# Optimization experiments

Hardware: AMD Instinct MI355X
Metric: run time of the kernel (lower is better)

The kernel has to match this reference:

```python
import jax, jax.numpy as jnp
from jax import lax
import numpy as np

T, B, D, H = 1024, 512, 128, 128  # time steps, batch, input dim, hidden size


def setup_inputs() -> dict:
    key = jax.random.key(0)
    ks = jax.random.split(key, 8)
    s_fc = 1.0 / np.sqrt(D)
    s_gru = 1.0 / np.sqrt(H)
    return {
        "x": jax.random.normal(ks[0], (T, B, D), dtype=jnp.float32),
        "W1": jax.random.uniform(ks[1], (128, D), jnp.float32, -s_fc, s_fc),
        "b1": jax.random.uniform(ks[2], (128,), jnp.float32, -s_fc, s_fc),
        "W_ih": jax.random.uniform(ks[3], (3 * H, 128), jnp.float32, -s_gru, s_gru),
        "W_hh": jax.random.uniform(ks[4], (3 * H, H), jnp.float32, -s_gru, s_gru),
        "b_ih": jax.random.uniform(ks[5], (3 * H,), jnp.float32, -s_gru, s_gru),
        "b_hh": jax.random.uniform(ks[6], (3 * H,), jnp.float32, -s_gru, s_gru),
    }


def reference(x, W1, b1, W_ih, W_hh, b_ih, b_hh):
    # fc1 applied to every step (batched once over T*B for efficiency)
    feats = jnp.einsum('tbd,hd->tbh', x, W1) + b1  # [T, B, 128]

    hidden = W_hh.shape[1]

    def step(h, f):
        # PyTorch GRUCell gate math
        gi = f @ W_ih.T + b_ih          # [B, 3H]
        gh = h @ W_hh.T + b_hh          # [B, 3H]
        i_r, i_z, i_n = jnp.split(gi, 3, axis=-1)
        h_r, h_z, h_n = jnp.split(gh, 3, axis=-1)
        r = jax.nn.sigmoid(i_r + h_r)
        z = jax.nn.sigmoid(i_z + h_z)
        n = jnp.tanh(i_n + r * h_n)
        h_new = (1.0 - z) * n + z * h
        return h_new, None

    # first call gru(feats) passes no hidden -> zeros initial state
    h0 = jnp.zeros((x.shape[1], hidden), dtype=x.dtype)
    h_final, _ = lax.scan(step, h0, feats)
    return h_final  # [B, H]
```

## Files before the change

### kernel.cpp

```cpp
#include <hip/hip_runtime.h>
#include <hip/hip_bf16.h>

#define T_STEPS 1024
#define BATCH   512
#define DIM     128
#define G3      384
#define NCHUNK  (T_STEPS/8)

typedef __attribute__((ext_vector_type(8))) short bf16x8;
typedef __attribute__((ext_vector_type(4))) float f32x4;

__device__ __forceinline__ short f2bf(float f) {
  unsigned u = __builtin_bit_cast(unsigned, f);
  u += 0x7FFFu + ((u >> 16) & 1u);
  return (short)(u >> 16);
}

__device__ __forceinline__ void block_sync_lds() {
  asm volatile("s_waitcnt lgkmcnt(0)\n\ts_barrier" ::: "memory");
}

__global__ void prep_kernel(const float* __restrict__ W1, const float* __restrict__ b1,
                            const float* __restrict__ W_ih, const float* __restrict__ W_hh,
                            const float* __restrict__ b_ih,
                            short* __restrict__ wc_bf, short* __restrict__ whh_bf,
                            float* __restrict__ bc) {
  const int g = blockIdx.x;
  const int d = threadIdx.x;
  float acc = 0.f;
  #pragma unroll 4
  for (int k = 0; k < 128; ++k)
    acc = fmaf(W_ih[g * 128 + k], W1[k * 128 + d], acc);
  wc_bf[g * 128 + d]  = f2bf(acc);
  whh_bf[g * 128 + d] = f2bf(W_hh[g * 128 + d]);

  __shared__ float red[128];
  red[d] = W_ih[g * 128 + d] * b1[d];
  __syncthreads();
  #pragma unroll
  for (int s = 64; s > 0; s >>= 1) {
    if (d < s) red[d] += red[d + s];
    __syncthreads();
  }
  if (d == 0) bc[g] = red[0] + b_ih[g];
}

__device__ __forceinline__ float gate_h(float gir, float giz, float gin,
                                        float ghr, float ghz, float ghn,
                                        float bhn, float hp) {
  const float r = __builtin_amdgcn_rcpf(1.f + __expf(-(gir + ghr)));
  const float z = __builtin_amdgcn_rcpf(1.f + __expf(-(giz + ghz)));
  float nv = gin + r * (ghn + bhn);
  nv = fminf(fmaxf(nv, -15.f), 15.f);
  const float e = __expf(2.f * nv);
  const float n = 1.f - 2.f * __builtin_amdgcn_rcpf(e + 1.f);
  return z * (hp - n) + n;
}

__global__ __launch_bounds__(512, 2) void gru_kernel(
    const float* __restrict__ x,
    const float* __restrict__ b_hh,
    const short* __restrict__ wc_bf,
    const short* __restrict__ whh_bf,
    const float* __restrict__ bc,
    float* __restrict__ out)
{
  const int tid = threadIdx.x;
  const int w   = tid >> 6;
  const int l   = tid & 63;
  const int q   = l >> 4;
  const int c   = l & 15;
  const int b0  = blockIdx.x * 2;

  __shared__ f32x4 gi4[2][16][128];
  __shared__ short hbuf[2][2][128];

  const f32x4 zero4 = {0.f, 0.f, 0.f, 0.f};

  if (w < 4) {
    const int half = q & 1;
    const int ch   = q >> 1;
    const int colX = w * 32 + (half << 4) + c;

    bf16x8 Bh[3][2][4];
    #pragma unroll
    for (int g = 0; g < 3; ++g)
      #pragma unroll
      for (int Tt = 0; Tt < 2; ++Tt)
        #pragma unroll
        for (int kt = 0; kt < 4; ++kt)
          Bh[g][Tt][kt] = *(const bf16x8*)(whh_bf +
              (g * 128 + w * 32 + Tt * 16 + c) * 128 + kt * 32 + q * 8);
    const float bhn = b_hh[256 + colX];

    ((short*)hbuf)[tid] = 0;
    float hp = 0.f;
    __syncthreads();

    const short* hb0 = &hbuf[0][c >> 3][q * 8];
    const short* hb1 = &hbuf[1][c >> 3][q * 8];

    for (int cc = 0; cc < NCHUNK; ++cc) {
      f32x4 gi[8];
      {
        const f32x4* gp = &gi4[cc & 1][ch][colX];
        #pragma unroll
        for (int s = 0; s < 8; ++s) gi[s] = gp[2 * s * 128];
      }
      #pragma unroll
      for (int s = 0; s < 8; ++s) {
        const short* hb = (s & 1) ? hb1 : hb0;
        bf16x8 Ah[4];
        #pragma unroll
        for (int kt = 0; kt < 4; ++kt)
          Ah[kt] = *(const bf16x8*)(hb + kt * 32);

        f32x4 a0[3] = {zero4, zero4, zero4};
        f32x4 a1[3] = {zero4, zero4, zero4};
        #pragma unroll
        for (int kt = 0; kt < 4; ++kt)
          #pragma unroll
          for (int g = 0; g < 3; ++g) {
            a0[g] = __builtin_amdgcn_mfma_f32_16x16x32_bf16(Ah[kt], Bh[g][0][kt], a0[g], 0, 0, 0);
            a1[g] = __builtin_amdgcn_mfma_f32_16x16x32_bf16(Ah[kt], Bh[g][1][kt], a1[g], 0, 0, 0);
          }
        const float ghr = half ? a1[0][0] : a0[0][0];
        const float ghz = half ? a1[1][0] : a0[1][0];
        const float ghn = half ? a1[2][0] : a0[2][0];
        const float h = gate_h(gi[s][0], gi[s][1], gi[s][2], ghr, ghz, ghn, bhn, hp);
        hp = h;
        hbuf[(s & 1) ^ 1][ch][colX] = f2bf(h);
        block_sync_lds();
      }
    }
    out[(size_t)(b0 + ch) * DIM + colX] = hp;
  } else {
    const int w4 = w - 4;
    const int jg0 = w4 * 32 + c, jg1 = jg0 + 16;
    bf16x8 Bc[3][2][4];
    #pragma unroll
    for (int g = 0; g < 3; ++g)
      #pragma unroll
      for (int Tt = 0; Tt < 2; ++Tt)
        #pragma unroll
        for (int kt = 0; kt < 4; ++kt)
          Bc[g][Tt][kt] = *(const bf16x8*)(wc_bf +
              (g * 128 + w4 * 32 + Tt * 16 + c) * 128 + kt * 32 + q * 8);
    const float fr0 = bc[jg0]       + b_hh[jg0];
    const float fz0 = bc[128 + jg0] + b_hh[128 + jg0];
    const float fn0 = bc[256 + jg0];
    const float fr1 = bc[jg1]       + b_hh[jg1];
    const float fz1 = bc[128 + jg1] + b_hh[128 + jg1];
    const float fn1 = bc[256 + jg1];

    const int trel = c >> 1, chn = c & 1;
    f32x4 xv[8];

    {
      const float* xb = x + ((size_t)trel * BATCH + (b0 + chn)) * DIM + q * 8;
      f32x4 xt[8];
      #pragma unroll
      for (int kt = 0; kt < 4; ++kt) {
        xt[2 * kt]     = *(const f32x4*)(xb + kt * 32);
        xt[2 * kt + 1] = *(const f32x4*)(xb + kt * 32 + 4);
      }
      bf16x8 Ax[4];
      #pragma unroll
      for (int kt = 0; kt < 4; ++kt) {
        const f32x4 v0 = xt[2 * kt], v1 = xt[2 * kt + 1];
        bf16x8 a;
        a[0] = f2bf(v0[0]); a[1] = f2bf(v0[1]); a[2] = f2bf(v0[2]); a[3] = f2bf(v0[3]);
        a[4] = f2bf(v1[0]); a[5] = f2bf(v1[1]); a[6] = f2bf(v1[2]); a[7] = f2bf(v1[3]);
        Ax[kt] = a;
      }
      f32x4 ga[2][3] = {{zero4, zero4, zero4}, {zero4, zero4, zero4}};
      #pragma unroll
      for (int kt = 0; kt < 4; ++kt)
        #pragma unroll
        for (int g = 0; g < 3; ++g) {
          ga[0][g] = __builtin_amdgcn_mfma_f32_16x16x32_bf16(Ax[kt], Bc[g][0][kt], ga[0][g], 0, 0, 0);
          ga[1][g] = __builtin_amdgcn_mfma_f32_16x16x32_bf16(Ax[kt], Bc[g][1][kt], ga[1][g], 0, 0, 0);
        }
      #pragma unroll
      for (int r = 0; r < 4; ++r) {
        f32x4 vA = {ga[0][0][r] + fr0, ga[0][1][r] + fz0, ga[0][2][r] + fn0, 0.f};
        f32x4 vB = {ga[1][0][r] + fr1, ga[1][1][r] + fz1, ga[1][2][r] + fn1, 0.f};
        gi4[0][4 * q + r][jg0] = vA;
        gi4[0][4 * q + r][jg1] = vB;
      }
      const float* xb1 = x + ((size_t)(8 + trel) * BATCH + (b0 + chn)) * DIM + q * 8;
      #pragma unroll
      for (int kt = 0; kt < 4; ++kt) {
        xv[2 * kt]     = *(const f32x4*)(xb1 + kt * 32);
        xv[2 * kt + 1] = *(const f32x4*)(xb1 + kt * 32 + 4);
      }
    }
    __syncthreads();

    for (int cc = 0; cc < NCHUNK; ++cc) {
      const int tc = cc + 1;
      bf16x8 Ax[4];
      f32x4 ga[2][3];
      #pragma unroll
      for (int s = 0; s < 8; ++s) {
        if (tc < NCHUNK) {
          if (s == 0) {
            #pragma unroll
            for (int kt = 0; kt < 4; ++kt) {
              const f32x4 v0 = xv[2 * kt], v1 = xv[2 * kt + 1];
              bf16x8 a;
              a[0] = f2bf(v0[0]); a[1] = f2bf(v0[1]); a[2] = f2bf(v0[2]); a[3] = f2bf(v0[3]);
              a[4] = f2bf(v1[0]); a[5] = f2bf(v1[1]); a[6] = f2bf(v1[2]); a[7] = f2bf(v1[3]);
              Ax[kt] = a;
            }
            #pragma unroll
            for (int Tt = 0; Tt < 2; ++Tt)
              #pragma unroll
              for (int g = 0; g < 3; ++g) ga[Tt][g] = zero4;
          } else if (s <= 4) {
            const int kt = s - 1;
            #pragma unroll
            for (int g = 0; g < 3; ++g) {
              ga[0][g] = __builtin_amdgcn_mfma_f32_16x16x32_bf16(Ax[kt], Bc[g][0][kt], ga[0][g], 0, 0, 0);
              ga[1][g] = __builtin_amdgcn_mfma_f32_16x16x32_bf16(Ax[kt], Bc[g][1][kt], ga[1][g], 0, 0, 0);
            }
          } else if (s == 5) {
            if (tc + 1 < NCHUNK) {
              const float* xb = x + ((size_t)((tc + 1) * 8 + trel) * BATCH + (b0 + chn)) * DIM + q * 8;
              #pragma unroll
              for (int kt = 0; kt < 4; ++kt) {
                xv[2 * kt]     = *(const f32x4*)(xb + kt * 32);
                xv[2 * kt + 1] = *(const f32x4*)(xb + kt * 32 + 4);
              }
            }
          } else if (s == 6) {
            #pragma unroll
            for (int r = 0; r < 4; ++r) {
              ga[0][0][r] += fr0; ga[0][1][r] += fz0; ga[0][2][r] += fn0;
              ga[1][0][r] += fr1; ga[1][1][r] += fz1; ga[1][2][r] += fn1;
            }
          } else {
            const int nbuf = tc & 1;
            #pragma unroll
            for (int r = 0; r < 4; ++r) {
              f32x4 vA = {ga[0][0][r], ga[0][1][r], ga[0][2][r], 0.f};
              f32x4 vB = {ga[1][0][r], ga[1][1][r], ga[1][2][r], 0.f};
              gi4[nbuf][4 * q + r][jg0] = vA;
              gi4[nbuf][4 * q + r][jg1] = vB;
            }
          }
        }
        block_sync_lds();
      }
    }
  }
}

extern "C" void kernel_launch(void* const* d_in, const int* in_sizes, int n_in,
                              void* d_out, int out_size, void* d_ws, size_t ws_size,
                              hipStream_t stream) {
  const float* x    = (const float*)d_in[0];
  const float* W1   = (const float*)d_in[1];
  const float* b1   = (const float*)d_in[2];
  const float* W_ih = (const float*)d_in[3];
  const float* W_hh = (const float*)d_in[4];
  const float* b_ih = (const float*)d_in[5];
  const float* b_hh = (const float*)d_in[6];
  float* out = (float*)d_out;

  char* ws = (char*)d_ws;
  short* wc_bf  = (short*)(ws);
  short* whh_bf = (short*)(ws + 98304);
  float* bc     = (float*)(ws + 196608);

  prep_kernel<<<dim3(G3), dim3(128), 0, stream>>>(W1, b1, W_ih, W_hh, b_ih, wc_bf, whh_bf, bc);
  gru_kernel<<<dim3(BATCH / 2), dim3(512), 0, stream>>>(x, b_hh, wc_bf, whh_bf, bc, out);
}
```

Measured before the change: 687.5 us.

## Fold log2e scaling into weights, split MFMA chains, pad LDS, raise recurrent priority

```diff
diff --git a/kernel.cpp b/kernel.cpp
--- a/kernel.cpp
+++ b/kernel.cpp
@@ -6,9 +6,14 @@
 #define DIM     128
 #define G3      384
 #define NCHUNK  (T_STEPS/8)
+#define GI_STRIDE 129
 
 typedef __attribute__((ext_vector_type(8))) short bf16x8;
 typedef __attribute__((ext_vector_type(4))) float f32x4;
+
+#define LOG2E  1.44269504f
+#define LOG2E2 2.88539008f
+#define NV_CLAMP 43.28f
 
 __device__ __forceinline__ short f2bf(float f) {
   unsigned u = __builtin_bit_cast(unsigned, f);
@@ -22,17 +27,18 @@
 
 __global__ void prep_kernel(const float* __restrict__ W1, const float* __restrict__ b1,
                             const float* __restrict__ W_ih, const float* __restrict__ W_hh,
-                            const float* __restrict__ b_ih,
+                            const float* __restrict__ b_ih, const float* __restrict__ b_hh,
                             short* __restrict__ wc_bf, short* __restrict__ whh_bf,
-                            float* __restrict__ bc) {
+                            float* __restrict__ bc, float* __restrict__ bhh_s) {
   const int g = blockIdx.x;
   const int d = threadIdx.x;
+  const float sg = (g < 256) ? LOG2E : LOG2E2;
   float acc = 0.f;
   #pragma unroll 4
   for (int k = 0; k < 128; ++k)
     acc = fmaf(W_ih[g * 128 + k], W1[k * 128 + d], acc);
-  wc_bf[g * 128 + d]  = f2bf(acc);
-  whh_bf[g * 128 + d] = f2bf(W_hh[g * 128 + d]);
+  wc_bf[g * 128 + d]  = f2bf(acc * sg);
+  whh_bf[g * 128 + d] = f2bf(W_hh[g * 128 + d] * sg);
 
   __shared__ float red[128];
   red[d] = W_ih[g * 128 + d] * b1[d];
@@ -42,24 +48,15 @@
     if (d < s) red[d] += red[d + s];
     __syncthreads();
   }
-  if (d == 0) bc[g] = red[0] + b_ih[g];
-}
-
-__device__ __forceinline__ float gate_h(float gir, float giz, float gin,
-                                        float ghr, float ghz, float ghn,
-                                        float bhn, float hp) {
-  const float r = __builtin_amdgcn_rcpf(1.f + __expf(-(gir + ghr)));
-  const float z = __builtin_amdgcn_rcpf(1.f + __expf(-(giz + ghz)));
-  float nv = gin + r * (ghn + bhn);
-  nv = fminf(fmaxf(nv, -15.f), 15.f);
-  const float e = __expf(2.f * nv);
-  const float n = 1.f - 2.f * __builtin_amdgcn_rcpf(e + 1.f);
-  return z * (hp - n) + n;
+  if (d == 0) {
+    bc[g]    = (red[0] + b_ih[g]) * sg;
+    bhh_s[g] = b_hh[g] * sg;
+  }
 }
 
 __global__ __launch_bounds__(512, 2) void gru_kernel(
     const float* __restrict__ x,
-    const float* __restrict__ b_hh,
+    const float* __restrict__ bhh_s,
     const short* __restrict__ wc_bf,
     const short* __restrict__ whh_bf,
     const float* __restrict__ bc,
@@ -72,7 +69,7 @@
   const int c   = l & 15;
   const int b0  = blockIdx.x * 2;
 
-  __shared__ f32x4 gi4[2][16][128];
+  __shared__ f32x4 gi4[2 * 16 * GI_STRIDE];
   __shared__ short hbuf[2][2][128];
 
   const f32x4 zero4 = {0.f, 0.f, 0.f, 0.f};
@@ -91,7 +88,7 @@
         for (int kt = 0; kt < 4; ++kt)
           Bh[g][Tt][kt] = *(const bf16x8*)(whh_bf +
               (g * 128 + w * 32 + Tt * 16 + c) * 128 + kt * 32 + q * 8);
-    const float bhn = b_hh[256 + colX];
+    const float bhn = bhh_s[256 + colX];
 
     ((short*)hbuf)[tid] = 0;
     float hp = 0.f;
@@ -100,12 +97,13 @@
     const short* hb0 = &hbuf[0][c >> 3][q * 8];
     const short* hb1 = &hbuf[1][c >> 3][q * 8];
 
+    __builtin_amdgcn_s_setprio(1);
     for (int cc = 0; cc < NCHUNK; ++cc) {
       f32x4 gi[8];
       {
-        const f32x4* gp = &gi4[cc & 1][ch][colX];
-        #pragma unroll
-        for (int s = 0; s < 8; ++s) gi[s] = gp[2 * s * 128];
+        const f32x4* gp = gi4 + (cc & 1) * (16 * GI_STRIDE) + ch * GI_STRIDE + colX;
+        #pragma unroll
+        for (int s = 0; s < 8; ++s) gi[s] = gp[2 * s * GI_STRIDE];
       }
       #pragma unroll
       for (int s = 0; s < 8; ++s) {
@@ -115,24 +113,49 @@
         for (int kt = 0; kt < 4; ++kt)
           Ah[kt] = *(const bf16x8*)(hb + kt * 32);
 
-        f32x4 a0[3] = {zero4, zero4, zero4};
-        f32x4 a1[3] = {zero4, zero4, zero4};
-        #pragma unroll
-        for (int kt = 0; kt < 4; ++kt)
-          #pragma unroll
-          for (int g = 0; g < 3; ++g) {
-            a0[g] = __builtin_amdgcn_mfma_f32_16x16x32_bf16(Ah[kt], Bh[g][0][kt], a0[g], 0, 0, 0);
-            a1[g] = __builtin_amdgcn_mfma_f32_16x16x32_bf16(Ah[kt], Bh[g][1][kt], a1[g], 0, 0, 0);
-          }
-        const float ghr = half ? a1[0][0] : a0[0][0];
-        const float ghz = half ? a1[1][0] : a0[1][0];
-        const float ghn = half ? a1[2][0] : a0[2][0];
-        const float h = gate_h(gi[s][0], gi[s][1], gi[s][2], ghr, ghz, ghn, bhn, hp);
+        f32x4 r0A = __builtin_amdgcn_mfma_f32_16x16x32_bf16(Ah[0], Bh[0][0][0], zero4, 0, 0, 0);
+        f32x4 r1A = __builtin_amdgcn_mfma_f32_16x16x32_bf16(Ah[0], Bh[0][1][0], zero4, 0, 0, 0);
+        f32x4 r0B = __builtin_amdgcn_mfma_f32_16x16x32_bf16(Ah[2], Bh[0][0][2], zero4, 0, 0, 0);
+        f32x4 r1B = __builtin_amdgcn_mfma_f32_16x16x32_bf16(Ah[2], Bh[0][1][2], zero4, 0, 0, 0);
+        r0A = __builtin_amdgcn_mfma_f32_16x16x32_bf16(Ah[1], Bh[0][0][1], r0A, 0, 0, 0);
+        r1A = __builtin_amdgcn_mfma_f32_16x16x32_bf16(Ah[1], Bh[0][1][1], r1A, 0, 0, 0);
+        r0B = __builtin_amdgcn_mfma_f32_16x16x32_bf16(Ah[3], Bh[0][0][3], r0B, 0, 0, 0);
+        r1B = __builtin_amdgcn_mfma_f32_16x16x32_bf16(Ah[3], Bh[0][1][3], r1B, 0, 0, 0);
+        f32x4 z0A = __builtin_amdgcn_mfma_f32_16x16x32_bf16(Ah[0], Bh[1][0][0], zero4, 0, 0, 0);
+        f32x4 z1A = __builtin_amdgcn_mfma_f32_16x16x32_bf16(Ah[0], Bh[1][1][0], zero4, 0, 0, 0);
+        f32x4 z0B = __builtin_amdgcn_mfma_f32_16x16x32_bf16(Ah[2], Bh[1][0][2], zero4, 0, 0, 0);
+        f32x4 z1B = __builtin_amdgcn_mfma_f32_16x16x32_bf16(Ah[2], Bh[1][1][2], zero4, 0, 0, 0);
+        z0A = __builtin_amdgcn_mfma_f32_16x16x32_bf16(Ah[1], Bh[1][0][1], z0A, 0, 0, 0);
+        z1A = __builtin_amdgcn_mfma_f32_16x16x32_bf16(Ah[1], Bh[1][1][1], z1A, 0, 0, 0);
+        z0B = __builtin_amdgcn_mfma_f32_16x16x32_bf16(Ah[3], Bh[1][0][3], z0B, 0, 0, 0);
+        z1B = __builtin_amdgcn_mfma_f32_16x16x32_bf16(Ah[3], Bh[1][1][3], z1B, 0, 0, 0);
+
+        const float ghr = half ? (r1A[0] + r1B[0]) : (r0A[0] + r0B[0]);
+        const float ghz = half ? (z1A[0] + z1B[0]) : (z0A[0] + z0B[0]);
+        const float rg = __builtin_amdgcn_rcpf(1.f + __builtin_amdgcn_exp2f(-(gi[s][0] + ghr)));
+        const float zg = __builtin_amdgcn_rcpf(1.f + __builtin_amdgcn_exp2f(-(gi[s][1] + ghz)));
+
+        f32x4 n0A = __builtin_amdgcn_mfma_f32_16x16x32_bf16(Ah[0], Bh[2][0][0], zero4, 0, 0, 0);
+        f32x4 n1A = __builtin_amdgcn_mfma_f32_16x16x32_bf16(Ah[0], Bh[2][1][0], zero4, 0, 0, 0);
+        f32x4 n0B = __builtin_amdgcn_mfma_f32_16x16x32_bf16(Ah[2], Bh[2][0][2], zero4, 0, 0, 0);
+        f32x4 n1B = __builtin_amdgcn_mfma_f32_16x16x32_bf16(Ah[2], Bh[2][1][2], zero4, 0, 0, 0);
+        n0A = __builtin_amdgcn_mfma_f32_16x16x32_bf16(Ah[1], Bh[2][0][1], n0A, 0, 0, 0);
+        n1A = __builtin_amdgcn_mfma_f32_16x16x32_bf16(Ah[1], Bh[2][1][1], n1A, 0, 0, 0);
+        n0B = __builtin_amdgcn_mfma_f32_16x16x32_bf16(Ah[3], Bh[2][0][3], n0B, 0, 0, 0);
+        n1B = __builtin_amdgcn_mfma_f32_16x16x32_bf16(Ah[3], Bh[2][1][3], n1B, 0, 0, 0);
+        const float ghn = half ? (n1A[0] + n1B[0]) : (n0A[0] + n0B[0]);
+
+        float nv = gi[s][2] + rg * (ghn + bhn);
+        nv = fminf(fmaxf(nv, -NV_CLAMP), NV_CLAMP);
+        const float e  = __builtin_amdgcn_exp2f(nv);
+        const float nn = 1.f - 2.f * __builtin_amdgcn_rcpf(e + 1.f);
+        const float h  = zg * (hp - nn) + nn;
         hp = h;
         hbuf[(s & 1) ^ 1][ch][colX] = f2bf(h);
         block_sync_lds();
       }
     }
+    __builtin_amdgcn_s_setprio(0);
     out[(size_t)(b0 + ch) * DIM + colX] = hp;
   } else {
     const int w4 = w - 4;
@@ -146,11 +169,11 @@
         for (int kt = 0; kt < 4; ++kt)
           Bc[g][Tt][kt] = *(const bf16x8*)(wc_bf +
               (g * 128 + w4 * 32 + Tt * 16 + c) * 128 + kt * 32 + q * 8);
-    const float fr0 = bc[jg0]       + b_hh[jg0];
-    const float fz0 = bc[128 + jg0] + b_hh[128 + jg0];
+    const float fr0 = bc[jg0]       + bhh_s[jg0];
+    const float fz0 = bc[128 + jg0] + bhh_s[128 + jg0];
     const float fn0 = bc[256 + jg0];
-    const float fr1 = bc[jg1]       + b_hh[jg1];
-    const float fz1 = bc[128 + jg1] + b_hh[128 + jg1];
+    const float fr1 = bc[jg1]       + bhh_s[jg1];
+    const float fz1 = bc[128 + jg1] + bhh_s[128 + jg1];
     const float fn1 = bc[256 + jg1];
 
     const int trel = c >> 1, chn = c & 1;
@@ -173,9 +196,14 @@
         a[4] = f2bf(v1[0]); a[5] = f2bf(v1[1]); a[6] = f2bf(v1[2]); a[7] = f2bf(v1[3]);
         Ax[kt] = a;
       }
-      f32x4 ga[2][3] = {{zero4, zero4, zero4}, {zero4, zero4, zero4}};
-      #pragma unroll
-      for (int kt = 0; kt < 4; ++kt)
+      f32x4 ga[2][3];
+      #pragma unroll
+      for (int g = 0; g < 3; ++g) {
+        ga[0][g] = __builtin_amdgcn_mfma_f32_16x16x32_bf16(Ax[0], Bc[g][0][0], zero4, 0, 0, 0);
+        ga[1][g] = __builtin_amdgcn_mfma_f32_16x16x32_bf16(Ax[0], Bc[g][1][0], zero4, 0, 0, 0);
+      }
+      #pragma unroll
+      for (int kt = 1; kt < 4; ++kt)
         #pragma unroll
         for (int g = 0; g < 3; ++g) {
           ga[0][g] = __builtin_amdgcn_mfma_f32_16x16x32_bf16(Ax[kt], Bc[g][0][kt], ga[0][g], 0, 0, 0);
@@ -185,8 +213,8 @@
       for (int r = 0; r < 4; ++r) {
         f32x4 vA = {ga[0][0][r] + fr0, ga[0][1][r] + fz0, ga[0][2][r] + fn0, 0.f};
         f32x4 vB = {ga[1][0][r] + fr1, ga[1][1][r] + fz1, ga[1][2][r] + fn1, 0.f};
-        gi4[0][4 * q + r][jg0] = vA;
-        gi4[0][4 * q + r][jg1] = vB;
+        gi4[(4 * q + r) * GI_STRIDE + jg0] = vA;
+        gi4[(4 * q + r) * GI_STRIDE + jg1] = vB;
       }
       const float* xb1 = x + ((size_t)(8 + trel) * BATCH + (b0 + chn)) * DIM + q * 8;
       #pragma unroll
@@ -213,10 +241,12 @@
               a[4] = f2bf(v1[0]); a[5] = f2bf(v1[1]); a[6] = f2bf(v1[2]); a[7] = f2bf(v1[3]);
               Ax[kt] = a;
             }
-            #pragma unroll
-            for (int Tt = 0; Tt < 2; ++Tt)
-              #pragma unroll
-              for (int g = 0; g < 3; ++g) ga[Tt][g] = zero4;
+          } else if (s == 1) {
+            #pragma unroll
+            for (int g = 0; g < 3; ++g) {
+              ga[0][g] = __builtin_amdgcn_mfma_f32_16x16x32_bf16(Ax[0], Bc[g][0][0], zero4, 0, 0, 0);
+              ga[1][g] = __builtin_amdgcn_mfma_f32_16x16x32_bf16(Ax[0], Bc[g][1][0], zero4, 0, 0, 0);
+            }
           } else if (s <= 4) {
             const int kt = s - 1;
             #pragma unroll
@@ -240,13 +270,13 @@
               ga[1][0][r] += fr1; ga[1][1][r] += fz1; ga[1][2][r] += fn1;
             }
           } else {
-            const int nbuf = tc & 1;
+            f32x4* gb = gi4 + (tc & 1) * (16 * GI_STRIDE);
             #pragma unroll
             for (int r = 0; r < 4; ++r) {
               f32x4 vA = {ga[0][0][r], ga[0][1][r], ga[0][2][r], 0.f};
               f32x4 vB = {ga[1][0][r], ga[1][1][r], ga[1][2][r], 0.f};
-              gi4[nbuf][4 * q + r][jg0] = vA;
-              gi4[nbuf][4 * q + r][jg1] = vB;
+              gb[(4 * q + r) * GI_STRIDE + jg0] = vA;
+              gb[(4 * q + r) * GI_STRIDE + jg1] = vB;
             }
           }
         }
@@ -272,7 +302,9 @@
   short* wc_bf  = (short*)(ws);
   short* whh_bf = (short*)(ws + 98304);
   float* bc     = (float*)(ws + 196608);
-
-  prep_kernel<<<dim3(G3), dim3(128), 0, stream>>>(W1, b1, W_ih, W_hh, b_ih, wc_bf, whh_bf, bc);
-  gru_kernel<<<dim3(BATCH / 2), dim3(512), 0, stream>>>(x, b_hh, wc_bf, whh_bf, bc, out);
-}
+  float* bhh_s  = (float*)(ws + 198144);
+
+  prep_kernel<<<dim3(G3), dim3(128), 0, stream>>>(W1, b1, W_ih, W_hh, b_ih, b_hh,
+                                                  wc_bf, whh_bf, bc, bhh_s);
+  gru_kernel<<<dim3(BATCH / 2), dim3(512), 0, stream>>>(x, bhh_s, wc_bf, whh_bf, bc, out);
+}
```

Measured after the change: 680.9 us. Within noise of the previous version (-1.0%).
